# Performance work log

Hardware: AMD Instinct MI355X
Metric: run time of the kernel (lower is better)

## Reference

```python
import math
import jax, jax.numpy as jnp
import numpy as np

N, S, E, H = 8, 1024, 768, 12  # batch, seq_len, n_embed, n_head


def setup_inputs() -> dict:
    key = jax.random.key(0)
    ks = jax.random.split(key, 10)
    s = 1.0 / math.sqrt(E)
    x = jax.random.normal(ks[0], (N, S, E), dtype=jnp.float32)
    # per-head full-width projections, stacked over heads: [H, E, E] (Linear weight layout [out, in])
    Wq = jax.random.normal(ks[1], (H, E, E), dtype=jnp.float32) * s
    Wk = jax.random.normal(ks[2], (H, E, E), dtype=jnp.float32) * s
    Wv = jax.random.normal(ks[3], (H, E, E), dtype=jnp.float32) * s
    bq = jax.random.normal(ks[4], (H, E), dtype=jnp.float32) * s
    bk = jax.random.normal(ks[5], (H, E), dtype=jnp.float32) * s
    bv = jax.random.normal(ks[6], (H, E), dtype=jnp.float32) * s
    Wc = jax.random.normal(ks[7], (E, H * E), dtype=jnp.float32) * (1.0 / math.sqrt(H * E))
    bc = jax.random.normal(ks[8], (E,), dtype=jnp.float32) * s
    return {"x": x, "Wq": Wq, "bq": bq, "Wk": Wk, "bk": bk, "Wv": Wv, "bv": bv, "Wc": Wc, "bc": bc}


def reference(x, Wq, bq, Wk, bk, Wv, bv, Wc, bc):
    # Full-width QKV per head: [H, N, S, E]
    q = jnp.einsum('nse,hde->hnsd', x, Wq) + bq[:, None, None, :]
    k = jnp.einsum('nse,hde->hnsd', x, Wk) + bk[:, None, None, :]
    v = jnp.einsum('nse,hde->hnsd', x, Wv) + bv[:, None, None, :]
    # scores scaled by sqrt(n_embed) (source quirk: full n_embed, not head_dim)
    scores = jnp.einsum('hnsd,hntd->hnst', q, k) / math.sqrt(E)
    causal = jnp.tril(jnp.ones((S, S), dtype=bool))
    scores = jnp.where(causal[None, None, :, :], scores, -jnp.inf)
    # dropout applied before softmax in source; p=0 (eval) -> identity
    attn = jax.nn.softmax(scores, axis=-1)
    heads = jnp.einsum('hnst,hntd->hnsd', attn, v)  # [H, N, S, E]
    concat = jnp.transpose(heads, (1, 2, 0, 3)).reshape(N, S, H * E)
    return concat @ Wc.T + bc
```

## Files before the change

### kernel.cpp

```cpp
#include <hip/hip_runtime.h>
#include <hip/hip_bf16.h>
#include <stdint.h>

#define SEQ    1024
#define NBAT   8
#define EMB    768
#define NHEAD  12
#define MROWS  (NBAT*SEQ)
#define SCALE_S 0.03608439182435161f

typedef unsigned short u16;
typedef __attribute__((ext_vector_type(8))) short bf16x8;
typedef __attribute__((ext_vector_type(4))) float f32x4;

typedef void __attribute__((address_space(1)))* gas_ptr;
typedef void __attribute__((address_space(3)))* las_ptr;

__device__ __forceinline__ void gload16(const void* g, void* l) {
  __builtin_amdgcn_global_load_lds((gas_ptr)(void*)g, (las_ptr)l, 16, 0, 0);
}

#define VMCNT0 asm volatile("s_waitcnt vmcnt(0)" ::: "memory")
#define VMCNT2 asm volatile("s_waitcnt vmcnt(2)" ::: "memory")
#define VMCNT4 asm volatile("s_waitcnt vmcnt(4)" ::: "memory")
#define LGKM0  asm volatile("s_waitcnt lgkmcnt(0)" ::: "memory")
#define BARRIER asm volatile("s_barrier" ::: "memory")

__device__ __forceinline__ u16 f2bf(float f) {
  union { float f; uint32_t u; } a; a.f = f;
  uint32_t r = a.u + 0x7fffu + ((a.u >> 16) & 1u);
  return (u16)(r >> 16);
}
__device__ __forceinline__ float bf2f(u16 b) {
  union { uint32_t u; float f; } c; c.u = (uint32_t)b << 16; return c.f;
}
__device__ __forceinline__ uint32_t pack2(float a, float b) {
  return (uint32_t)f2bf(a) | ((uint32_t)f2bf(b) << 16);
}

__global__ void k_cvt(const float* __restrict__ s, u16* __restrict__ d, long n) {
  long i = ((long)blockIdx.x*blockDim.x + threadIdx.x)*8;
  if (i >= n) return;
  float4 a = *(const float4*)(s+i);
  float4 b = *(const float4*)(s+i+4);
  uint4 o; o.x = pack2(a.x,a.y); o.y = pack2(a.z,a.w);
  o.z = pack2(b.x,b.y); o.w = pack2(b.z,b.w);
  *(uint4*)(d+i) = o;
}

__global__ void k_cvtT(const float* __restrict__ wq, const float* __restrict__ wk,
                       u16* __restrict__ dq, u16* __restrict__ dk, int Gi) {
  __shared__ float t[64][65];
  int z = blockIdx.z;
  const float* src = (z < Gi) ? wq + (size_t)z*EMB*EMB : wk + (size_t)(z-Gi)*EMB*EMB;
  u16* dst = (z < Gi) ? dq + (size_t)z*EMB*EMB : dk + (size_t)(z-Gi)*EMB*EMB;
  int d0 = blockIdx.x*64, e0 = blockIdx.y*64;
  int tt = threadIdx.x;
  int el = tt & 63, db = tt >> 6;
  #pragma unroll
  for (int p = 0; p < 16; ++p) {
    int dl = p*4 + db;
    t[dl][el] = src[(size_t)(d0+dl)*EMB + e0 + el];
  }
  __syncthreads();
  int dl2 = tt & 63, eb = tt >> 6;
  #pragma unroll
  for (int p = 0; p < 16; ++p) {
    int e2 = p*4 + eb;
    dst[(size_t)(e0+e2)*EMB + d0 + dl2] = f2bf(t[dl2][e2]);
  }
}

__global__ void k_cvtwc(const float* __restrict__ wc, u16* __restrict__ d, int Gi, int h0) {
  long ncol = (long)Gi*EMB;
  long i = ((long)blockIdx.x*blockDim.x + threadIdx.x)*4;
  if (i >= 768*ncol) return;
  long eo = i / ncol, c = i - eo*ncol;
  long g = c / EMB, dd = c - g*EMB;
  const float* s = wc + eo*(long)(NHEAD*EMB) + (h0+g)*EMB + dd;
  float4 a = *(const float4*)s;
  uint2 o; o.x = pack2(a.x,a.y); o.y = pack2(a.z,a.w);
  *(uint2*)(d+i) = o;
}

__global__ void k_mka(const u16* __restrict__ wkT, const float* __restrict__ bq,
                      float* __restrict__ a) {
  int g = blockIdx.y;
  int e = blockIdx.x*256 + threadIdx.x;
  const u16* row = wkT + (size_t)g*EMB*EMB + (size_t)e*EMB;
  const float* b = bq + (size_t)g*EMB;
  float s = 0.f;
  for (int d = 0; d < EMB; ++d) s += bf2f(row[d]) * b[d];
  a[(size_t)g*EMB + e] = s;
}

__global__ void k_mkv(const u16* __restrict__ xb, const float* __restrict__ a,
                      float* __restrict__ v) {
  int g = blockIdx.y;
  int w = threadIdx.x >> 6, l = threadIdx.x & 63;
  int i = blockIdx.x*8 + w;
  const u16* xr = xb + (size_t)i*EMB;
  const float* ag = a + (size_t)g*EMB;
  float s = 0.f;
  #pragma unroll
  for (int c = 0; c < 12; ++c) {
    int e = c*64 + l;
    s += bf2f(xr[e]) * ag[e];
  }
  s += __shfl_xor(s, 1); s += __shfl_xor(s, 2); s += __shfl_xor(s, 4);
  s += __shfl_xor(s, 8); s += __shfl_xor(s, 16); s += __shfl_xor(s, 32);
  if (l == 0) v[(size_t)g*MROWS + i] = s;
}

struct Gemm256Args {
  const u16* A; int lda;
  const u16* B; int ldb; int K;
  u16* Cb; long c_hs; int ldc;
  const float* bias; const float* bias2;
  int gsplit; int mode; int swap;
};

__global__ __launch_bounds__(512, 2) void k_gemm256d(Gemm256Args p0, Gemm256Args p1)
{
  __shared__ u16 lsA[2*16384];
  __shared__ u16 lsB[2*16384];

  const Gemm256Args P = blockIdx.z ? p1 : p0;
  int m0 = (P.swap ? blockIdx.y : blockIdx.x) * 256;
  int n0 = (P.swap ? blockIdx.x : blockIdx.y) * 256;
  int tid = threadIdx.x;
  int w = tid >> 6, l = tid & 63;
  int wr = w >> 2, wc = w & 3;

  const u16* gA = P.A + (size_t)(m0 + 32*w + (l>>3))*P.lda + (((l&7) ^ (l>>3)) << 3);
  const u16* gB = P.B + (size_t)(n0 + 32*w + (l>>3))*P.ldb + (((l&7) ^ (l>>3)) << 3);

#define STAGE256(t, buf) do { \
    int k0_ = (t)*64; \
    _Pragma("unroll") \
    for (int c_ = 0; c_ < 4; ++c_) \
      gload16(gA + (size_t)(c_*8)*P.lda + k0_, lsA + (buf)*16384 + (32*w + 8*c_)*64); \
    _Pragma("unroll") \
    for (int c_ = 0; c_ < 4; ++c_) \
      gload16(gB + (size_t)(c_*8)*P.ldb + k0_, lsB + (buf)*16384 + (32*w + 8*c_)*64); \
  } while(0)

  f32x4 acc[8][4];
  #pragma unroll
  for (int i = 0; i < 8; ++i)
    #pragma unroll
    for (int j = 0; j < 4; ++j) acc[i][j] = (f32x4)0.0f;

  int nt = P.K >> 6;
  STAGE256(0, 0);
  for (int t = 0; t < nt; ++t) {
    VMCNT0; BARRIER;
    if (t + 1 < nt) STAGE256(t+1, (t+1)&1);
    const u16* la = lsA + (t&1)*16384;
    const u16* lb = lsB + (t&1)*16384;
    #pragma unroll
    for (int ks = 0; ks < 2; ++ks) {
      int off = (((4*ks + (l>>4)) ^ (l&7)) << 3);
      bf16x8 af[8], bf_[4];
      #pragma unroll
      for (int fi = 0; fi < 8; ++fi)
        af[fi] = *(const bf16x8*)(la + (wr*128 + fi*16 + (l&15))*64 + off);
      #pragma unroll
      for (int fj = 0; fj < 4; ++fj)
        bf_[fj] = *(const bf16x8*)(lb + (wc*64 + fj*16 + (l&15))*64 + off);
      __builtin_amdgcn_s_setprio(1);
      #pragma unroll
      for (int fi = 0; fi < 8; ++fi)
        #pragma unroll
        for (int fj = 0; fj < 4; ++fj)
          acc[fi][fj] = __builtin_amdgcn_mfma_f32_16x16x32_bf16(af[fi], bf_[fj], acc[fi][fj], 0, 0, 0);
      __builtin_amdgcn_s_setprio(0);
    }
  }
#undef STAGE256

  if (P.mode == 0) {
    int s = n0 / 768;
    int dbase = n0 - s*768 + wc*64;
    const float* bsl = P.bias ? ((s < P.gsplit) ? P.bias + (size_t)s*768
                                                : P.bias2 + (size_t)(s - P.gsplit)*768)
                              : (const float*)0;
    u16* Cs = P.Cb + (size_t)s*P.c_hs;
    #pragma unroll
    for (int fj = 0; fj < 4; ++fj) {
      int dcol = dbase + fj*16 + (l&15);
      float bb = bsl ? bsl[dcol] : 0.f;
      #pragma unroll
      for (int fi = 0; fi < 8; ++fi) {
        #pragma unroll
        for (int r = 0; r < 4; ++r) {
          int row = m0 + wr*128 + fi*16 + (l>>4)*4 + r;
          Cs[(size_t)row*768 + dcol] = f2bf(acc[fi][fj][r] + bb);
        }
      }
    }
  } else {
    #pragma unroll
    for (int fi = 0; fi < 8; ++fi) {
      #pragma unroll
      for (int r = 0; r < 4; ++r) {
        int row = m0 + wr*128 + fi*16 + (l>>4)*4 + r;
        float bb = P.bias[row];
        #pragma unroll
        for (int fj = 0; fj < 4; ++fj) {
          int cbn = n0 + wc*64 + fj*16 + (l&15);
          P.Cb[(size_t)row*P.ldc + cbn] = f2bf(acc[fi][fj][r] + bb);
        }
      }
    }
  }
}

__global__ __launch_bounds__(256) void k_gemm(
    const u16* __restrict__ A, long a_hs, int lda,
    const u16* __restrict__ B, long b_hs, int ldb, int K,
    u16* Cb, float* Cf, long c_hs, int ldc,
    const float* __restrict__ bias, const float* __restrict__ bias2,
    long bias_hs, int gsplit, int mode, int swapxy)
{
  __shared__ u16 lsA[3*4096];
  __shared__ u16 lsB[3*4096];
  int g = blockIdx.z;
  const u16* Ag = A + (long)g*a_hs;
  const u16* Bg = B + (long)g*b_hs;
  int tm = swapxy ? blockIdx.y : blockIdx.x;
  int tn = swapxy ? blockIdx.x : blockIdx.y;
  int m0 = tm*128, n0 = tn*128;
  int tid = threadIdx.x;
  int w = tid >> 6, l = tid & 63;

  int srow = l >> 2;
  int scol = ((l & 3) ^ ((l >> 3) & 3)) * 8;
  const u16* ga0 = Ag + (long)(m0 + (2*w)*16   + srow)*lda + scol;
  const u16* ga1 = Ag + (long)(m0 + (2*w+1)*16 + srow)*lda + scol;
  const u16* gb0 = Bg + (long)(n0 + (2*w)*16   + srow)*ldb + scol;
  const u16* gb1 = Bg + (long)(n0 + (2*w+1)*16 + srow)*ldb + scol;

#define GSTAGE(k0, buf) do { \
    gload16(ga0 + (k0), lsA + (buf)*4096 + (2*w)*512); \
    gload16(ga1 + (k0), lsA + (buf)*4096 + (2*w+1)*512); \
    gload16(gb0 + (k0), lsB + (buf)*4096 + (2*w)*512); \
    gload16(gb1 + (k0), lsB + (buf)*4096 + (2*w+1)*512); \
  } while(0)

  f32x4 acc[4][4];
  #pragma unroll
  for (int i = 0; i < 4; ++i)
    #pragma unroll
    for (int j = 0; j < 4; ++j) acc[i][j] = (f32x4)0.0f;

  int wr = w >> 1, wc_ = w & 1;
  int frow = l & 15;
  int sp = (l >> 4) ^ ((frow >> 1) & 3);
  int aoff[4], boff[4];
  #pragma unroll
  for (int i = 0; i < 4; ++i) {
    aoff[i] = (wr*64 + i*16 + frow)*32 + sp*8;
    boff[i] = (wc_*64 + i*16 + frow)*32 + sp*8;
  }

  int nt = K >> 5;
  GSTAGE(0, 0);
  GSTAGE(32, 1);
  VMCNT4; BARRIER;
  int cur = 0;
  for (int t = 0; t < nt; ++t) {
    if (t + 2 < nt) {
      int nb = cur + 2; if (nb >= 3) nb -= 3;
      GSTAGE((t+2) << 5, nb);
    }
    const u16* la = lsA + cur*4096;
    const u16* lb = lsB + cur*4096;
    bf16x8 af[4], bfr[4];
    #pragma unroll
    for (int i = 0; i < 4; ++i) af[i] = *(const bf16x8*)(la + aoff[i]);
    #pragma unroll
    for (int j = 0; j < 4; ++j) bfr[j] = *(const bf16x8*)(lb + boff[j]);
    #pragma unroll
    for (int i = 0; i < 4; ++i)
      #pragma unroll
      for (int j = 0; j < 4; ++j)
        acc[i][j] = __builtin_amdgcn_mfma_f32_16x16x32_bf16(af[i], bfr[j], acc[i][j], 0, 0, 0);
    if (t + 2 < nt) { VMCNT4; } else { VMCNT0; }
    LGKM0; BARRIER;
    cur = (cur == 2) ? 0 : cur + 1;
  }
#undef GSTAGE

  u16* Cbg = Cb ? Cb + (long)g*c_hs : (u16*)0;
  const float* bsel = (g < gsplit) ? bias : bias2;
  long gi = (g < gsplit) ? g : g - gsplit;
  const float* bs = bsel ? bsel + gi*bias_hs : (const float*)0;
  int rl = (l >> 4)*4, cl = l & 15;
  #pragma unroll
  for (int i = 0; i < 4; ++i) {
    #pragma unroll
    for (int j = 0; j < 4; ++j) {
      int rb = m0 + wr*64 + i*16 + rl;
      int cb = n0 + wc_*64 + j*16 + cl;
      float cbv = 0.f;
      if ((mode == 0 || mode == 2) && bs) cbv = bs[cb];
      #pragma unroll
      for (int r = 0; r < 4; ++r) {
        int rr = rb + r;
        float v = acc[i][j][r];
        v += (mode == 1) ? bs[rr] : cbv;
        size_t idx = (size_t)rr*(size_t)ldc + cb;
        if (mode <= 1) Cbg[idx] = f2bf(v);
        else if (mode == 2) Cf[idx] = v;
        else Cf[idx] += v;
      }
    }
  }
}

__global__ __launch_bounds__(512, 2) void k_attn(
    const u16* __restrict__ qb, const u16* __restrict__ xkb,
    const u16* __restrict__ vtb, const float* __restrict__ vh,
    u16* __restrict__ hb, int ldh)
{
  __shared__ u16 kls[3*8192];
  __shared__ u16 vls[3*8192];
  __shared__ float s_t[64*68];
  __shared__ u16 p_t[64*64];
  __shared__ float e_s[64];

  int b = blockIdx.x;
  int xcd = b & 7, kk_ = b >> 3;
  int gn = xcd + 8*(kk_ >> 3), pair = kk_ & 7;
  int g = gn >> 3, n = gn & 7;

  const u16* Q  = qb  + (size_t)g*MROWS*EMB + (size_t)n*SEQ*EMB;
  const u16* Kp = xkb + (size_t)n*SEQ*EMB;
  const u16* Vt = vtb + (size_t)g*EMB*MROWS + (size_t)n*SEQ;
  const float* Vh = vh + (size_t)g*MROWS + (size_t)n*SEQ;
  u16* H = hb + (size_t)(n*SEQ)*ldh + (size_t)g*EMB;

  int tid = threadIdx.x;
  int w = tid >> 6, l = tid & 63;
  int qg = w >> 1;
  int cg = w & 1;
  int frow = l & 15;
  int fsw = frow & 7;
  int srow = tid >> 3;
  int sphys = tid & 7;
  int scol = ((sphys ^ (srow & 7)) << 3);

#define KSTAGE(base, pc, buf) do { \
    gload16((base) + (pc)*128,      kls + (buf)*8192 + w*512); \
    gload16((base) + (pc)*128 + 64, kls + (buf)*8192 + 4096 + w*512); \
  } while(0)
#define VSTAGE(vc, buf) do { \
    gload16(Vs + (size_t)((vc)*128)*MROWS,      vls + (buf)*8192 + w*512); \
    gload16(Vs + (size_t)((vc)*128 + 64)*MROWS, vls + (buf)*8192 + 4096 + w*512); \
  } while(0)

  for (int half = 0; half < 2; ++half) {
    int qt = half ? 15 - pair : pair;
    int q0 = qt * 64;
    int nt = qt + 1;

    f32x4 acc[6][4];
    #pragma unroll
    for (int i = 0; i < 6; ++i)
      #pragma unroll
      for (int j = 0; j < 4; ++j) acc[i][j] = (f32x4)0.0f;
    float m_reg = -1e30f, l_reg = 0.f;

    const u16* Qs = Q + (size_t)(q0 + srow)*EMB + scol;
    bf16x8 qreg[12][2];
    KSTAGE(Qs, 0, 0);
    KSTAGE(Qs, 1, 1);
    VMCNT2; BARRIER;
    #pragma unroll
    for (int pc = 0; pc < 6; ++pc) {
      if (pc < 4) KSTAGE(Qs, pc+2, (pc+2)%3);
      const u16* qb_ = kls + (pc%3)*8192;
      #pragma unroll
      for (int kk2 = 0; kk2 < 2; ++kk2)
        #pragma unroll
        for (int kkl = 0; kkl < 2; ++kkl)
          qreg[2*pc + kk2][kkl] = *(const bf16x8*)(qb_ + kk2*4096 + (qg*16 + frow)*64
                                                   + (((kkl*4 + (l>>4)) ^ fsw) << 3));
      if (pc < 4) { VMCNT2; } else if (pc == 4) { VMCNT0; }
      LGKM0; BARRIER;
    }

    for (int tt = 0; tt < nt; ++tt) {
      int t0 = tt*64;
      const u16* Ks = Kp + (size_t)(t0 + srow)*EMB + scol;
      const u16* Vs = Vt + (size_t)srow*MROWS + t0 + scol;
      float vv0 = Vh[t0 + cg*32 + frow];
      float vv1 = Vh[t0 + cg*32 + 16 + frow];
      if (tt == 0) { KSTAGE(Ks, 0, 0); KSTAGE(Ks, 1, 1); }
      VMCNT2; BARRIER;

      f32x4 sacc[2]; sacc[0] = (f32x4)0.0f; sacc[1] = (f32x4)0.0f;
      #pragma unroll
      for (int c = 0; c < 6; ++c) {
        if (c < 4)       KSTAGE(Ks, c+2, (c+2)%3);
        else if (c == 4) VSTAGE(0, 0);
        else             VSTAGE(1, 1);
        const u16* kb_ = kls + (c%3)*8192;
        __builtin_amdgcn_s_setprio(1);
        #pragma unroll
        for (int kk2 = 0; kk2 < 2; ++kk2) {
          #pragma unroll
          for (int kkl = 0; kkl < 2; ++kkl) {
            int so = ((kkl*4 + (l>>4)) ^ fsw) << 3;
            bf16x8 aq = qreg[2*c + kk2][kkl];
            #pragma unroll
            for (int cc = 0; cc < 2; ++cc) {
              bf16x8 bk_ = *(const bf16x8*)(kb_ + kk2*4096 + ((cg*2 + cc)*16 + frow)*64 + so);
              sacc[cc] = __builtin_amdgcn_mfma_f32_16x16x32_bf16(aq, bk_, sacc[cc], 0, 0, 0);
            }
          }
        }
        __builtin_amdgcn_s_setprio(0);
        if (c < 5) { VMCNT2; LGKM0; BARRIER; }
      }

      #pragma unroll
      for (int r = 0; r < 4; ++r) {
        s_t[(qg*16 + (l>>4)*4 + r)*68 + cg*32 + frow]      = (sacc[0][r] + vv0)*SCALE_S;
        s_t[(qg*16 + (l>>4)*4 + r)*68 + cg*32 + 16 + frow] = (sacc[1][r] + vv1)*SCALE_S;
      }
      LGKM0; BARRIER;
      {
        int qglob = q0 + srow;
        int cbase = t0 + sphys*8;
        float v[8]; float mx = -1e30f;
        #pragma unroll
        for (int j = 0; j < 8; ++j) {
          float s = s_t[srow*68 + sphys*8 + j];
          if (cbase + j > qglob) s = -1e30f;
          v[j] = s; mx = fmaxf(mx, s);
        }
        mx = fmaxf(mx, __shfl_xor(mx, 1));
        mx = fmaxf(mx, __shfl_xor(mx, 2));
        mx = fmaxf(mx, __shfl_xor(mx, 4));
        float mn = fmaxf(m_reg, mx);
        float esc = __expf(m_reg - mn);
        float ps = 0.f; u16 pk[8];
        #pragma unroll
        for (int j = 0; j < 8; ++j) { float p = __expf(v[j] - mn); ps += p; pk[j] = f2bf(p); }
        ps += __shfl_xor(ps, 1); ps += __shfl_xor(ps, 2); ps += __shfl_xor(ps, 4);
        l_reg = l_reg*esc + ps; m_reg = mn;
        if (sphys == 0) e_s[srow] = esc;
        uint4 pv;
        pv.x = (uint32_t)pk[0] | ((uint32_t)pk[1] << 16);
        pv.y = (uint32_t)pk[2] | ((uint32_t)pk[3] << 16);
        pv.z = (uint32_t)pk[4] | ((uint32_t)pk[5] << 16);
        pv.w = (uint32_t)pk[6] | ((uint32_t)pk[7] << 16);
        *(uint4*)(p_t + srow*64 + ((sphys ^ (srow & 7)) << 3)) = pv;
      }
      VMCNT2; LGKM0; BARRIER;
      float er[4];
      #pragma unroll
      for (int r = 0; r < 4; ++r) er[r] = e_s[qg*16 + (l>>4)*4 + r];
      #pragma unroll
      for (int i = 0; i < 6; ++i)
        #pragma unroll
        for (int j = 0; j < 4; ++j)
          #pragma unroll
          for (int r = 0; r < 4; ++r) acc[i][j][r] *= er[r];
      bf16x8 pa[2];
      #pragma unroll
      for (int kk = 0; kk < 2; ++kk)
        pa[kk] = *(const bf16x8*)(p_t + (qg*16 + frow)*64 + (((kk*4 + (l>>4)) ^ fsw) << 3));
      bool stage_next = (tt + 1 < nt);
      const u16* Ks2 = Kp + (size_t)(t0 + 64 + srow)*EMB + scol;
      #pragma unroll
      for (int c = 0; c < 6; ++c) {
        if (c < 4)            VSTAGE(c+2, (c+2)%3);
        else if (stage_next)  { if (c == 4) KSTAGE(Ks2, 0, 0); else KSTAGE(Ks2, 1, 1); }
        const u16* vb_ = vls + (c%3)*8192;
        __builtin_amdgcn_s_setprio(1);
        #pragma unroll
        for (int cf = 0; cf < 4; ++cf) {
          #pragma unroll
          for (int kk = 0; kk < 2; ++kk) {
            bf16x8 vbf = *(const bf16x8*)(vb_ + (cg*64 + cf*16 + frow)*64 + (((kk*4 + (l>>4)) ^ fsw) << 3));
            acc[c][cf] = __builtin_amdgcn_mfma_f32_16x16x32_bf16(pa[kk], vbf, acc[c][cf], 0, 0, 0);
          }
        }
        __builtin_amdgcn_s_setprio(0);
        if (c < 4)      { VMCNT2; LGKM0; BARRIER; }
        else if (c == 4){ if (stage_next) { VMCNT2; } else { VMCNT0; } LGKM0; BARRIER; }
      }
    }
    if (sphys == 0) e_s[srow] = l_reg;
    LGKM0; BARRIER;
    float linv[4];
    #pragma unroll
    for (int r = 0; r < 4; ++r) linv[r] = 1.0f / e_s[qg*16 + (l>>4)*4 + r];
    #pragma unroll
    for (int i = 0; i < 6; ++i)
      #pragma unroll
      for (int j = 0; j < 4; ++j) {
        int col = i*128 + cg*64 + j*16 + (l & 15);
        #pragma unroll
        for (int r = 0; r < 4; ++r) {
          int row = q0 + qg*16 + (l>>4)*4 + r;
          H[(size_t)row*ldh + col] = f2bf(acc[i][j][r]*linv[r]);
        }
      }
    BARRIER;
  }
#undef KSTAGE
#undef VSTAGE
}

extern "C" void kernel_launch(void* const* d_in, const int* in_sizes, int n_in,
                              void* d_out, int out_size, void* d_ws, size_t ws_size,
                              hipStream_t stream) {
  const float* x  = (const float*)d_in[0];
  const float* Wq = (const float*)d_in[1];
  const float* bq = (const float*)d_in[2];
  const float* Wk = (const float*)d_in[3];
  const float* bv = (const float*)d_in[6];
  const float* Wv = (const float*)d_in[5];
  const float* Wc = (const float*)d_in[7];
  const float* bc = (const float*)d_in[8];
  float* out = (float*)d_out;

  const size_t XB  = (size_t)MROWS*EMB*sizeof(u16);
  const size_t WHB = (size_t)EMB*EMB*sizeof(u16);
  const size_t VHB = (size_t)MROWS*sizeof(float);
  const size_t AB  = (size_t)EMB*sizeof(float);
  const size_t fixed = XB + 36*WHB + 12*(VHB + AB) + 8192;
  int G = 4;
  while (G > 2 && fixed + (size_t)G*3*XB > ws_size) --G;

  char* ws = (char*)d_ws;
  u16* xb  = (u16*)ws;  ws += XB;
  u16* wvb = (u16*)ws;  ws += 12*WHB;
  u16* wcb = (u16*)ws;  ws += 12*WHB;
  u16* mtb = (u16*)ws;  ws += 12*WHB;
  float* vh = (float*)ws; ws += 12*VHB;
  float* ab = (float*)ws; ws += 12*AB;
  u16* yb  = (u16*)ws;  ws += (size_t)G*XB;
  u16* vtb = (u16*)ws;  ws += (size_t)G*XB;
  u16* hbf = (u16*)ws;  ws += (size_t)G*XB;
  u16* wqT = hbf;
  u16* wkT = vtb;

  k_cvt<<<dim3(3072), dim3(256), 0, stream>>>(x, xb, (long)MROWS*EMB);
  k_cvtT<<<dim3(12, 12, 24), dim3(256), 0, stream>>>(Wq, Wk, wqT, wkT, 12);
  k_cvt<<<dim3((unsigned)((12L*EMB*EMB/8)/256)), dim3(256), 0, stream>>>(
      Wv, wvb, 12L*EMB*EMB);
  k_cvtwc<<<dim3((unsigned)((768L*12*EMB/4)/256)), dim3(256), 0, stream>>>(Wc, wcb, 12, 0);
  k_gemm<<<dim3(6, 6, 12), dim3(256), 0, stream>>>(
      wkT, (long)EMB*EMB, EMB, wqT, (long)EMB*EMB, EMB, EMB,
      mtb, (float*)0, (long)EMB*EMB, EMB,
      (const float*)0, (const float*)0, 0L, 9999, 0, 0);
  k_mka<<<dim3(3, 12), dim3(256), 0, stream>>>(wkT, bq, ab);
  k_mkv<<<dim3(1024, 12), dim3(512), 0, stream>>>(xb, ab, vh);

  for (int h0 = 0; h0 < NHEAD; h0 += G) {
    int Gi = (G < NHEAD - h0) ? G : (NHEAD - h0);
    Gemm256Args ay = { xb, EMB, mtb + (size_t)h0*EMB*EMB, EMB, EMB,
                       yb, (long)MROWS*EMB, 768,
                       (const float*)0, (const float*)0, Gi, 0, 0 };
    Gemm256Args av = { wvb + (size_t)h0*EMB*EMB, EMB, xb, EMB, EMB,
                       vtb, 0L, MROWS,
                       bv + (size_t)h0*EMB, (const float*)0, 9999, 1, 1 };
    k_gemm256d<<<dim3(32, 3*Gi, 2), dim3(512), 0, stream>>>(ay, av);
    k_attn<<<dim3(8*NBAT*Gi), dim3(512), 0, stream>>>(
        yb, xb, vtb, vh + (size_t)h0*MROWS, hbf, Gi*EMB);
    k_gemm<<<dim3(64, 6, 1), dim3(256), 0, stream>>>(
        hbf, 0L, Gi*EMB, wcb + (size_t)h0*EMB, 0L, NHEAD*EMB, Gi*EMB,
        (u16*)0, out, 0L, EMB,
        (h0 == 0 ? bc : (const float*)0), (const float*)0, 0L, 9999,
        (h0 == 0 ? 2 : 3), 0);
  }
}
```

Baseline: 1.009 ms.

## Split attention blocks into 32-row query tiles with 256 threads and double buffering

The attention kernel now launches twice as many workgroups of 256 threads, each handling 32 query rows instead of 64. The K/V shared-memory staging goes from triple to double buffering and the Q preload is reorganised to match. The aim is more concurrent workgroups per CU and better load balance across the causal triangle. In exchange, the K and V tiles are reloaded twice as often, and the full vmcnt(0) waits after every phase give up load/compute overlap.

```diff
diff --git a/kernel.cpp b/kernel.cpp
--- a/kernel.cpp
+++ b/kernel.cpp
@@ -23,6 +23,7 @@
 #define VMCNT0 asm volatile("s_waitcnt vmcnt(0)" ::: "memory")
 #define VMCNT2 asm volatile("s_waitcnt vmcnt(2)" ::: "memory")
 #define VMCNT4 asm volatile("s_waitcnt vmcnt(4)" ::: "memory")
+#define VMCNT6 asm volatile("s_waitcnt vmcnt(6)" ::: "memory")
 #define LGKM0  asm volatile("s_waitcnt lgkmcnt(0)" ::: "memory")
 #define BARRIER asm volatile("s_barrier" ::: "memory")
 
@@ -319,20 +320,21 @@
   }
 }
 
-__global__ __launch_bounds__(512, 2) void k_attn(
+__global__ __launch_bounds__(256, 2) void k_attn(
     const u16* __restrict__ qb, const u16* __restrict__ xkb,
     const u16* __restrict__ vtb, const float* __restrict__ vh,
     u16* __restrict__ hb, int ldh)
 {
-  __shared__ u16 kls[3*8192];
-  __shared__ u16 vls[3*8192];
-  __shared__ float s_t[64*68];
-  __shared__ u16 p_t[64*64];
-  __shared__ float e_s[64];
+  __shared__ u16 kls[2*8192];
+  __shared__ u16 vls[2*8192];
+  __shared__ float s_t[32*68];
+  __shared__ u16 p_t[32*64];
+  __shared__ float e_s[32];
 
   int b = blockIdx.x;
   int xcd = b & 7, kk_ = b >> 3;
-  int gn = xcd + 8*(kk_ >> 3), pair = kk_ & 7;
+  int pair = kk_ & 15;
+  int gn = xcd + 8*(kk_ >> 4);
   int g = gn >> 3, n = gn & 7;
 
   const u16* Q  = qb  + (size_t)g*MROWS*EMB + (size_t)n*SEQ*EMB;
@@ -347,23 +349,68 @@
   int cg = w & 1;
   int frow = l & 15;
   int fsw = frow & 7;
+  int hi = l >> 4;
   int srow = tid >> 3;
   int sphys = tid & 7;
   int scol = ((sphys ^ (srow & 7)) << 3);
 
 #define KSTAGE(base, pc, buf) do { \
-    gload16((base) + (pc)*128,      kls + (buf)*8192 + w*512); \
-    gload16((base) + (pc)*128 + 64, kls + (buf)*8192 + 4096 + w*512); \
+    const u16* s_ = (base) + (size_t)srow*EMB + (pc)*128 + scol; \
+    u16* d_ = kls + (buf)*8192 + w*512; \
+    gload16(s_,                  d_); \
+    gload16(s_ + (size_t)32*EMB, d_ + 2048); \
+    gload16(s_ + 64,                  d_ + 4096); \
+    gload16(s_ + (size_t)32*EMB + 64, d_ + 6144); \
   } while(0)
 #define VSTAGE(vc, buf) do { \
-    gload16(Vs + (size_t)((vc)*128)*MROWS,      vls + (buf)*8192 + w*512); \
-    gload16(Vs + (size_t)((vc)*128 + 64)*MROWS, vls + (buf)*8192 + 4096 + w*512); \
+    const u16* s_ = Vt + (size_t)((vc)*128 + srow)*MROWS + t0 + scol; \
+    u16* d_ = vls + (buf)*8192 + w*512; \
+    gload16(s_,                       d_); \
+    gload16(s_ + (size_t)32*MROWS,    d_ + 2048); \
+    gload16(s_ + (size_t)64*MROWS,    d_ + 4096); \
+    gload16(s_ + (size_t)96*MROWS,    d_ + 6144); \
+  } while(0)
+#define QSTAGE(pc, dst) do { \
+    const u16* s_ = Q + (size_t)(q0 + srow)*EMB + (pc)*128 + scol; \
+    gload16(s_,      (dst) + w*512); \
+    gload16(s_ + 64, (dst) + 2048 + w*512); \
+  } while(0)
+#define RD_Q(pc, src) do { \
+    _Pragma("unroll") for (int kk2 = 0; kk2 < 2; ++kk2) \
+      _Pragma("unroll") for (int kkl = 0; kkl < 2; ++kkl) \
+        qreg[2*(pc) + kk2][kkl] = *(const bf16x8*)((src) + kk2*2048 + (qg*16 + frow)*64 \
+                                                   + (((kkl*4 + hi) ^ fsw) << 3)); \
+  } while(0)
+#define QK_PH(c, buf) do { \
+    const u16* kb_ = kls + (buf)*8192; \
+    __builtin_amdgcn_s_setprio(1); \
+    _Pragma("unroll") for (int kk2 = 0; kk2 < 2; ++kk2) \
+      _Pragma("unroll") for (int kkl = 0; kkl < 2; ++kkl) { \
+        int so = ((kkl*4 + hi) ^ fsw) << 3; \
+        bf16x8 aq = qreg[2*(c) + kk2][kkl]; \
+        _Pragma("unroll") for (int cc = 0; cc < 2; ++cc) { \
+          bf16x8 bk_ = *(const bf16x8*)(kb_ + kk2*4096 + ((cg*2 + cc)*16 + frow)*64 + so); \
+          sacc[cc] = __builtin_amdgcn_mfma_f32_16x16x32_bf16(aq, bk_, sacc[cc], 0, 0, 0); \
+        } \
+      } \
+    __builtin_amdgcn_s_setprio(0); \
+  } while(0)
+#define PV_PH(c, buf) do { \
+    const u16* vb_ = vls + (buf)*8192; \
+    __builtin_amdgcn_s_setprio(1); \
+    _Pragma("unroll") for (int cf = 0; cf < 4; ++cf) \
+      _Pragma("unroll") for (int kk = 0; kk < 2; ++kk) { \
+        bf16x8 vbf = *(const bf16x8*)(vb_ + (cg*64 + cf*16 + frow)*64 + (((kk*4 + hi) ^ fsw) << 3)); \
+        acc[(c)][cf] = __builtin_amdgcn_mfma_f32_16x16x32_bf16(pa[kk], vbf, acc[(c)][cf], 0, 0, 0); \
+      } \
+    __builtin_amdgcn_s_setprio(0); \
   } while(0)
 
   for (int half = 0; half < 2; ++half) {
-    int qt = half ? 15 - pair : pair;
-    int q0 = qt * 64;
-    int nt = qt + 1;
+    int qt = half ? 31 - pair : pair;
+    int q0 = qt * 32;
+    int ntk = (qt >> 1) + 1;
+    int qglob = q0 + srow;
 
     f32x4 acc[6][4];
     #pragma unroll
@@ -372,67 +419,40 @@
       for (int j = 0; j < 4; ++j) acc[i][j] = (f32x4)0.0f;
     float m_reg = -1e30f, l_reg = 0.f;
 
-    const u16* Qs = Q + (size_t)(q0 + srow)*EMB + scol;
     bf16x8 qreg[12][2];
-    KSTAGE(Qs, 0, 0);
-    KSTAGE(Qs, 1, 1);
-    VMCNT2; BARRIER;
-    #pragma unroll
-    for (int pc = 0; pc < 6; ++pc) {
-      if (pc < 4) KSTAGE(Qs, pc+2, (pc+2)%3);
-      const u16* qb_ = kls + (pc%3)*8192;
-      #pragma unroll
-      for (int kk2 = 0; kk2 < 2; ++kk2)
-        #pragma unroll
-        for (int kkl = 0; kkl < 2; ++kkl)
-          qreg[2*pc + kk2][kkl] = *(const bf16x8*)(qb_ + kk2*4096 + (qg*16 + frow)*64
-                                                   + (((kkl*4 + (l>>4)) ^ fsw) << 3));
-      if (pc < 4) { VMCNT2; } else if (pc == 4) { VMCNT0; }
-      LGKM0; BARRIER;
-    }
-
-    for (int tt = 0; tt < nt; ++tt) {
+    VMCNT0;
+    QSTAGE(0, kls); QSTAGE(1, kls + 8192); QSTAGE(2, vls); QSTAGE(3, vls + 8192);
+    VMCNT6; BARRIER;
+    RD_Q(0, kls);          VMCNT4; LGKM0; BARRIER;
+    QSTAGE(4, kls);        RD_Q(1, kls + 8192); VMCNT4; LGKM0; BARRIER;
+    QSTAGE(5, kls + 8192); RD_Q(2, vls);        VMCNT4; LGKM0; BARRIER;
+    RD_Q(3, vls + 8192);   VMCNT2; LGKM0; BARRIER;
+    RD_Q(4, kls);          VMCNT0; LGKM0; BARRIER;
+    KSTAGE(Kp, 0, 0);      RD_Q(5, kls + 8192); VMCNT0; LGKM0; BARRIER;
+
+    for (int tt = 0; tt < ntk; ++tt) {
       int t0 = tt*64;
-      const u16* Ks = Kp + (size_t)(t0 + srow)*EMB + scol;
-      const u16* Vs = Vt + (size_t)srow*MROWS + t0 + scol;
+      const u16* Kb  = Kp + (size_t)t0*EMB;
+      const u16* Kbn = Kp + (size_t)(t0 + 64)*EMB;
+      bool sn = (tt + 1 < ntk);
       float vv0 = Vh[t0 + cg*32 + frow];
       float vv1 = Vh[t0 + cg*32 + 16 + frow];
-      if (tt == 0) { KSTAGE(Ks, 0, 0); KSTAGE(Ks, 1, 1); }
-      VMCNT2; BARRIER;
 
       f32x4 sacc[2]; sacc[0] = (f32x4)0.0f; sacc[1] = (f32x4)0.0f;
-      #pragma unroll
-      for (int c = 0; c < 6; ++c) {
-        if (c < 4)       KSTAGE(Ks, c+2, (c+2)%3);
-        else if (c == 4) VSTAGE(0, 0);
-        else             VSTAGE(1, 1);
-        const u16* kb_ = kls + (c%3)*8192;
-        __builtin_amdgcn_s_setprio(1);
-        #pragma unroll
-        for (int kk2 = 0; kk2 < 2; ++kk2) {
-          #pragma unroll
-          for (int kkl = 0; kkl < 2; ++kkl) {
-            int so = ((kkl*4 + (l>>4)) ^ fsw) << 3;
-            bf16x8 aq = qreg[2*c + kk2][kkl];
-            #pragma unroll
-            for (int cc = 0; cc < 2; ++cc) {
-              bf16x8 bk_ = *(const bf16x8*)(kb_ + kk2*4096 + ((cg*2 + cc)*16 + frow)*64 + so);
-              sacc[cc] = __builtin_amdgcn_mfma_f32_16x16x32_bf16(aq, bk_, sacc[cc], 0, 0, 0);
-            }
-          }
-        }
-        __builtin_amdgcn_s_setprio(0);
-        if (c < 5) { VMCNT2; LGKM0; BARRIER; }
+      KSTAGE(Kb, 1, 1);  QK_PH(0, 0);  VMCNT0; BARRIER;
+      KSTAGE(Kb, 2, 0);  QK_PH(1, 1);  VMCNT0; BARRIER;
+      KSTAGE(Kb, 3, 1);  QK_PH(2, 0);  VMCNT0; BARRIER;
+      KSTAGE(Kb, 4, 0);  QK_PH(3, 1);  VMCNT0; BARRIER;
+      KSTAGE(Kb, 5, 1);  QK_PH(4, 0);  VMCNT0; BARRIER;
+      VSTAGE(0, 0);      QK_PH(5, 1);
+      #pragma unroll
+      for (int r = 0; r < 4; ++r) {
+        s_t[(qg*16 + hi*4 + r)*68 + cg*32 + frow]      = (sacc[0][r] + vv0)*SCALE_S;
+        s_t[(qg*16 + hi*4 + r)*68 + cg*32 + 16 + frow] = (sacc[1][r] + vv1)*SCALE_S;
       }
-
-      #pragma unroll
-      for (int r = 0; r < 4; ++r) {
-        s_t[(qg*16 + (l>>4)*4 + r)*68 + cg*32 + frow]      = (sacc[0][r] + vv0)*SCALE_S;
-        s_t[(qg*16 + (l>>4)*4 + r)*68 + cg*32 + 16 + frow] = (sacc[1][r] + vv1)*SCALE_S;
-      }
-      LGKM0; BARRIER;
+      VMCNT0; LGKM0; BARRIER;
+      VSTAGE(1, 1);
       {
-        int qglob = q0 + srow;
         int cbase = t0 + sphys*8;
         float v[8]; float mx = -1e30f;
         #pragma unroll
@@ -459,10 +479,10 @@
         pv.w = (uint32_t)pk[6] | ((uint32_t)pk[7] << 16);
         *(uint4*)(p_t + srow*64 + ((sphys ^ (srow & 7)) << 3)) = pv;
       }
-      VMCNT2; LGKM0; BARRIER;
+      LGKM0; BARRIER;
       float er[4];
       #pragma unroll
-      for (int r = 0; r < 4; ++r) er[r] = e_s[qg*16 + (l>>4)*4 + r];
+      for (int r = 0; r < 4; ++r) er[r] = e_s[qg*16 + hi*4 + r];
       #pragma unroll
       for (int i = 0; i < 6; ++i)
         #pragma unroll
@@ -472,33 +492,21 @@
       bf16x8 pa[2];
       #pragma unroll
       for (int kk = 0; kk < 2; ++kk)
-        pa[kk] = *(const bf16x8*)(p_t + (qg*16 + frow)*64 + (((kk*4 + (l>>4)) ^ fsw) << 3));
-      bool stage_next = (tt + 1 < nt);
-      const u16* Ks2 = Kp + (size_t)(t0 + 64 + srow)*EMB + scol;
-      #pragma unroll
-      for (int c = 0; c < 6; ++c) {
-        if (c < 4)            VSTAGE(c+2, (c+2)%3);
-        else if (stage_next)  { if (c == 4) KSTAGE(Ks2, 0, 0); else KSTAGE(Ks2, 1, 1); }
-        const u16* vb_ = vls + (c%3)*8192;
-        __builtin_amdgcn_s_setprio(1);
-        #pragma unroll
-        for (int cf = 0; cf < 4; ++cf) {
-          #pragma unroll
-          for (int kk = 0; kk < 2; ++kk) {
-            bf16x8 vbf = *(const bf16x8*)(vb_ + (cg*64 + cf*16 + frow)*64 + (((kk*4 + (l>>4)) ^ fsw) << 3));
-            acc[c][cf] = __builtin_amdgcn_mfma_f32_16x16x32_bf16(pa[kk], vbf, acc[c][cf], 0, 0, 0);
-          }
-        }
-        __builtin_amdgcn_s_setprio(0);
-        if (c < 4)      { VMCNT2; LGKM0; BARRIER; }
-        else if (c == 4){ if (stage_next) { VMCNT2; } else { VMCNT0; } LGKM0; BARRIER; }
-      }
+        pa[kk] = *(const bf16x8*)(p_t + (qg*16 + frow)*64 + (((kk*4 + hi) ^ fsw) << 3));
+      PV_PH(0, 0);       VMCNT0; BARRIER;
+      VSTAGE(2, 0);      PV_PH(1, 1);  VMCNT0; BARRIER;
+      VSTAGE(3, 1);      PV_PH(2, 0);  VMCNT0; BARRIER;
+      VSTAGE(4, 0);      PV_PH(3, 1);  VMCNT0; BARRIER;
+      VSTAGE(5, 1);      PV_PH(4, 0);  VMCNT0; BARRIER;
+      if (sn) KSTAGE(Kbn, 0, 0);
+      PV_PH(5, 1);       VMCNT0; BARRIER;
     }
+
     if (sphys == 0) e_s[srow] = l_reg;
     LGKM0; BARRIER;
     float linv[4];
     #pragma unroll
-    for (int r = 0; r < 4; ++r) linv[r] = 1.0f / e_s[qg*16 + (l>>4)*4 + r];
+    for (int r = 0; r < 4; ++r) linv[r] = 1.0f / e_s[qg*16 + hi*4 + r];
     #pragma unroll
     for (int i = 0; i < 6; ++i)
       #pragma unroll
@@ -506,7 +514,7 @@
         int col = i*128 + cg*64 + j*16 + (l & 15);
         #pragma unroll
         for (int r = 0; r < 4; ++r) {
-          int row = q0 + qg*16 + (l>>4)*4 + r;
+          int row = q0 + qg*16 + hi*4 + r;
           H[(size_t)row*ldh + col] = f2bf(acc[i][j][r]*linv[r]);
         }
       }
@@ -514,6 +522,10 @@
   }
 #undef KSTAGE
 #undef VSTAGE
+#undef QSTAGE
+#undef RD_Q
+#undef QK_PH
+#undef PV_PH
 }
 
 extern "C" void kernel_launch(void* const* d_in, const int* in_sizes, int n_in,
@@ -571,7 +583,7 @@
                        vtb, 0L, MROWS,
                        bv + (size_t)h0*EMB, (const float*)0, 9999, 1, 1 };
     k_gemm256d<<<dim3(32, 3*Gi, 2), dim3(512), 0, stream>>>(ay, av);
-    k_attn<<<dim3(8*NBAT*Gi), dim3(512), 0, stream>>>(
+    k_attn<<<dim3(16*NBAT*Gi), dim3(256), 0, stream>>>(
         yb, xb, vtb, vh + (size_t)h0*MROWS, hbf, Gi*EMB);
     k_gemm<<<dim3(64, 6, 1), dim3(256), 0, stream>>>(
         hbf, 0L, Gi*EMB, wcb + (size_t)h0*EMB, 0L, NHEAD*EMB, Gi*EMB,
```

New measurement: 1.139 ms. 12.9% more time.

## Fold previous group's output projection into next group's QKV GEMM launch

Applied to the files above, without the earlier changes.

The 256-tile GEMM kernel now takes a third argument set and picks among three problems by blockIdx.y. Each head group's launch also runs the previous group's output-projection GEMM (float output, bias on the first group, accumulate afterwards). Only the last group's projection still uses the separate small-tile GEMM. This cuts the number of launches and lets the projection fill the grid alongside the Y/V GEMMs, using the larger tile. In exchange it adds a float read-modify-write epilogue and per-block argument selection inside the kernel.

```diff
diff --git a/kernel.cpp b/kernel.cpp
--- a/kernel.cpp
+++ b/kernel.cpp
@@ -115,19 +115,23 @@
 struct Gemm256Args {
   const u16* A; int lda;
   const u16* B; int ldb; int K;
-  u16* Cb; long c_hs; int ldc;
+  u16* Cb; float* Cf; long c_hs; int ldc;
   const float* bias; const float* bias2;
-  int gsplit; int mode; int swap;
+  int gsplit; int mode; int swap; int ny;
 };
 
-__global__ __launch_bounds__(512, 2) void k_gemm256d(Gemm256Args p0, Gemm256Args p1)
+__global__ __launch_bounds__(512, 2) void k_gemm256t(Gemm256Args p0, Gemm256Args p1,
+                                                     Gemm256Args p2)
 {
   __shared__ u16 lsA[2*16384];
   __shared__ u16 lsB[2*16384];
 
-  const Gemm256Args P = blockIdx.z ? p1 : p0;
-  int m0 = (P.swap ? blockIdx.y : blockIdx.x) * 256;
-  int n0 = (P.swap ? blockIdx.x : blockIdx.y) * 256;
+  Gemm256Args P; int y = blockIdx.y;
+  if (y < p0.ny) { P = p0; }
+  else if (y < p0.ny + p1.ny) { P = p1; y -= p0.ny; }
+  else { P = p2; y -= p0.ny + p1.ny; }
+  int m0 = (P.swap ? y : (int)blockIdx.x) * 256;
+  int n0 = (P.swap ? (int)blockIdx.x : y) * 256;
   int tid = threadIdx.x;
   int w = tid >> 6, l = tid & 63;
   int wr = w >> 2, wc = w & 3;
@@ -199,7 +203,7 @@
         }
       }
     }
-  } else {
+  } else if (P.mode == 1) {
     #pragma unroll
     for (int fi = 0; fi < 8; ++fi) {
       #pragma unroll
@@ -210,6 +214,22 @@
         for (int fj = 0; fj < 4; ++fj) {
           int cbn = n0 + wc*64 + fj*16 + (l&15);
           P.Cb[(size_t)row*P.ldc + cbn] = f2bf(acc[fi][fj][r] + bb);
+        }
+      }
+    }
+  } else {
+    #pragma unroll
+    for (int fj = 0; fj < 4; ++fj) {
+      int col = n0 + wc*64 + fj*16 + (l&15);
+      float bb = (P.mode == 2 && P.bias) ? P.bias[col] : 0.f;
+      #pragma unroll
+      for (int fi = 0; fi < 8; ++fi) {
+        #pragma unroll
+        for (int r = 0; r < 4; ++r) {
+          int row = m0 + wr*128 + fi*16 + (l>>4)*4 + r;
+          size_t idx = (size_t)row*P.ldc + col;
+          if (P.mode == 2) P.Cf[idx] = acc[fi][fj][r] + bb;
+          else             P.Cf[idx] += acc[fi][fj][r];
         }
       }
     }
@@ -562,21 +582,36 @@
   k_mka<<<dim3(3, 12), dim3(256), 0, stream>>>(wkT, bq, ab);
   k_mkv<<<dim3(1024, 12), dim3(512), 0, stream>>>(xb, ab, vh);
 
+  int h_prev = -1, Gi_prev = 0;
   for (int h0 = 0; h0 < NHEAD; h0 += G) {
     int Gi = (G < NHEAD - h0) ? G : (NHEAD - h0);
-    Gemm256Args ay = { xb, EMB, mtb + (size_t)h0*EMB*EMB, EMB, EMB,
-                       yb, (long)MROWS*EMB, 768,
-                       (const float*)0, (const float*)0, Gi, 0, 0 };
-    Gemm256Args av = { wvb + (size_t)h0*EMB*EMB, EMB, xb, EMB, EMB,
-                       vtb, 0L, MROWS,
-                       bv + (size_t)h0*EMB, (const float*)0, 9999, 1, 1 };
-    k_gemm256d<<<dim3(32, 3*Gi, 2), dim3(512), 0, stream>>>(ay, av);
+    Gemm256Args ay; Gemm256Args av; Gemm256Args ap;
+    ay.A = xb; ay.lda = EMB; ay.B = mtb + (size_t)h0*EMB*EMB; ay.ldb = EMB; ay.K = EMB;
+    ay.Cb = yb; ay.Cf = 0; ay.c_hs = (long)MROWS*EMB; ay.ldc = 768;
+    ay.bias = 0; ay.bias2 = 0; ay.gsplit = Gi; ay.mode = 0; ay.swap = 0; ay.ny = 3*Gi;
+    av.A = wvb + (size_t)h0*EMB*EMB; av.lda = EMB; av.B = xb; av.ldb = EMB; av.K = EMB;
+    av.Cb = vtb; av.Cf = 0; av.c_hs = 0; av.ldc = MROWS;
+    av.bias = bv + (size_t)h0*EMB; av.bias2 = 0; av.gsplit = 9999; av.mode = 1;
+    av.swap = 1; av.ny = 3*Gi;
+    ap.A = 0; ap.lda = 0; ap.B = 0; ap.ldb = 0; ap.K = 64; ap.Cb = 0; ap.Cf = 0;
+    ap.c_hs = 0; ap.ldc = 0; ap.bias = 0; ap.bias2 = 0; ap.gsplit = 0; ap.mode = 3;
+    ap.swap = 0; ap.ny = 0;
+    if (h_prev >= 0) {
+      ap.A = hbf; ap.lda = Gi_prev*EMB;
+      ap.B = wcb + (size_t)h_prev*EMB; ap.ldb = NHEAD*EMB; ap.K = Gi_prev*EMB;
+      ap.Cf = out; ap.ldc = EMB;
+      ap.bias = (h_prev == 0) ? bc : (const float*)0;
+      ap.mode = (h_prev == 0) ? 2 : 3;
+      ap.ny = 3;
+    }
+    k_gemm256t<<<dim3(32, ay.ny + av.ny + ap.ny), dim3(512), 0, stream>>>(ay, av, ap);
     k_attn<<<dim3(8*NBAT*Gi), dim3(512), 0, stream>>>(
         yb, xb, vtb, vh + (size_t)h0*MROWS, hbf, Gi*EMB);
-    k_gemm<<<dim3(64, 6, 1), dim3(256), 0, stream>>>(
-        hbf, 0L, Gi*EMB, wcb + (size_t)h0*EMB, 0L, NHEAD*EMB, Gi*EMB,
-        (u16*)0, out, 0L, EMB,
-        (h0 == 0 ? bc : (const float*)0), (const float*)0, 0L, 9999,
-        (h0 == 0 ? 2 : 3), 0);
-  }
-}
+    h_prev = h0; Gi_prev = Gi;
+  }
+  k_gemm<<<dim3(64, 6, 1), dim3(256), 0, stream>>>(
+      hbf, 0L, Gi_prev*EMB, wcb + (size_t)h_prev*EMB, 0L, NHEAD*EMB, Gi_prev*EMB,
+      (u16*)0, out, 0L, EMB,
+      (h_prev == 0 ? bc : (const float*)0), (const float*)0, 0L, 9999,
+      (h_prev == 0 ? 2 : 3), 0);
+}
```

After: 1.056 ms. 4.7% more time.
